# Kernel optimization log

Measured on AMD Instinct MI355X. Metric: run time of the kernel, lower is better.

## Reference

```python
import jax, jax.numpy as jnp
import numpy as np

N_NODES = 100000
N_EDGES = 1600000
D = 128


def gcn_conv(x, src, dst, ew, W, b, num_nodes):
    """PyG GCNConv: self-loops (weight 1), symmetric deg^{-1/2} normalization,
    linear transform (no bias) then scatter-add aggregation at dst, bias after."""
    loop = jnp.arange(num_nodes)
    s = jnp.concatenate([src, loop])
    d = jnp.concatenate([dst, loop])
    w = jnp.concatenate([ew, jnp.ones((num_nodes,), dtype=x.dtype)])
    deg = jax.ops.segment_sum(w, d, num_segments=num_nodes)
    dinv = jnp.where(deg > 0, jax.lax.rsqrt(deg), 0.0).astype(x.dtype)
    norm = dinv[s] * w * dinv[d]                      # [E+N]
    h = x @ W                                          # [N, out]
    msgs = h[s] * norm[:, None]                        # [E+N, out]
    return jax.ops.segment_sum(msgs, d, num_segments=num_nodes) + b


def setup_inputs() -> dict:
    key = jax.random.key(0)
    ks = jax.random.split(key, 7)
    x = jax.random.normal(ks[0], (N_NODES, D), dtype=jnp.float32)
    edge_index = jax.random.randint(ks[1], (2, N_EDGES), 0, N_NODES, dtype=jnp.int64)
    edge_weight = jax.random.uniform(ks[2], (N_EDGES,), dtype=jnp.float32)
    scale = 1.0 / np.sqrt(D)
    W1 = jax.random.normal(ks[3], (D, D), dtype=jnp.float32) * scale
    b1 = jax.random.normal(ks[4], (D,), dtype=jnp.float32) * 0.01
    W2 = jax.random.normal(ks[5], (D, D), dtype=jnp.float32) * scale
    b2 = jax.random.normal(ks[6], (D,), dtype=jnp.float32) * 0.01
    return {"x": x, "edge_index": edge_index, "edge_weight": edge_weight,
            "W1": W1, "b1": b1, "W2": W2, "b2": b2}


def reference(x, edge_index, edge_weight, W1, b1, W2, b2):
    src, dst = edge_index[0], edge_index[1]
    n = x.shape[0]
    h = gcn_conv(x, src, dst, edge_weight, W1, b1, n)
    h = jax.nn.relu(h)
    h = gcn_conv(h, src, dst, edge_weight, W2, b2, n)
    return jax.nn.relu(h)
```

## Files before the change

### kernel.cpp

```cpp
#include <hip/hip_runtime.h>

#define D 128
#define CAP 64
#define NCELL 391
#define BN2 256
#define CELLCAP 4608
#define BCAP 16
#define ABLK 768

typedef __attribute__((ext_vector_type(8))) short bf16x8;
typedef __attribute__((ext_vector_type(4))) float f32x4;
typedef __attribute__((ext_vector_type(4))) uint  u32x4;
typedef __attribute__((ext_vector_type(2))) float f32x2;

__device__ __forceinline__ ushort f2bf(float f) {
    uint u = __float_as_uint(f);
    return (ushort)((u + 0x7FFFu + ((u >> 16) & 1u)) >> 16);
}

__global__ __launch_bounds__(256) void k_prep(const float* __restrict__ W1,
                                              const float* __restrict__ W2,
                                              ushort* __restrict__ Wt1,
                                              ushort* __restrict__ Wt2,
                                              int* scnt) {
    int i = blockIdx.x * 256 + threadIdx.x;
    if (i < NCELL) scnt[i] = 0;
    if (i < 2 * D * D) {
        const float* W = (i < D * D) ? W1 : W2;
        ushort* Wt     = (i < D * D) ? Wt1 : Wt2;
        int j = i & (D * D - 1);
        int k = j >> 7, nn = j & 127;
        Wt[nn * D + k] = f2bf(W[k * D + nn]);
    }
}

__global__ __launch_bounds__(256) void k_bin(const int* __restrict__ src,
                                             const int* __restrict__ dst,
                                             const float* __restrict__ ew,
                                             int* scnt,
                                             uint2* __restrict__ rec, int nE, int epb) {
    __shared__ uint2 lrec[NCELL * BCAP];
    __shared__ int   bcnt[NCELL];
    __shared__ int   gbase[NCELL];
    const int tid = threadIdx.x;

    for (int i = tid; i < NCELL; i += 256) bcnt[i] = 0;
    __syncthreads();

    int e0 = blockIdx.x * epb;
    int e1 = min(e0 + epb, nE);
    for (int e = e0 + tid; e < e1; e += 256) {
        int d = dst[e];
        uint q = (uint)__float2int_rn(ew[e] * 32767.0f);
        uint2 r = make_uint2(((uint)src[e] << 15) | q, (uint)(d & (BN2 - 1)));
        int cell = d >> 8;
        int p = atomicAdd(&bcnt[cell], 1);
        if (p < BCAP) {
            lrec[cell * BCAP + p] = r;
        } else {
            int gp = atomicAdd(&scnt[cell], 1);
            if (gp < CELLCAP) rec[(size_t)cell * CELLCAP + gp] = r;
        }
    }
    __syncthreads();

    const int offs = (blockIdx.x * 97) % NCELL;

    for (int i = tid; i < NCELL; i += 256) {
        int cell = i + offs; if (cell >= NCELL) cell -= NCELL;
        int c = min(bcnt[cell], BCAP);
        gbase[cell] = (c > 0) ? atomicAdd(&scnt[cell], c) : 0;
    }
    __syncthreads();

    const int wave = tid >> 6, lane = tid & 63;
    for (int i = wave; i < NCELL; i += 4) {
        int cell = i + offs; if (cell >= NCELL) cell -= NCELL;
        int c = min(bcnt[cell], BCAP);
        if (lane < c)
            rec[(size_t)cell * CELLCAP + gbase[cell] + lane] = lrec[cell * BCAP + lane];
    }
}

__global__ __launch_bounds__(256) void k_build(const uint2* __restrict__ rec,
                                               const int* __restrict__ scnt,
                                               uint* __restrict__ bucket,
                                               int* __restrict__ cnt,
                                               float* __restrict__ dinv, int n) {
    __shared__ uint rows[BN2 * (CAP + 1)];
    __shared__ int  lcnt[BN2];
    const int tid = threadIdx.x;
    const int b   = blockIdx.x;

    lcnt[tid] = 0;
    __syncthreads();

    int c = min(scnt[b], CELLCAP);
    for (int i = tid; i < c; i += 256) {
        uint2 r = rec[(size_t)b * CELLCAP + i];
        int nl = (int)r.y;
        int p = atomicAdd(&lcnt[nl], 1);
        if (p < CAP - 1) rows[nl * (CAP + 1) + p] = r.x;
    }
    __syncthreads();

    int node = b * BN2 + tid;
    int cc = min(lcnt[tid], CAP - 1);
    lcnt[tid] = cc;
    if (node < n) {
        float wsum = 0.f;
        for (int i = 0; i < cc; ++i)
            wsum += (float)(rows[tid * (CAP + 1) + i] & 32767u);
        dinv[node] = rsqrtf(1.0f + wsum * (1.0f / 32767.0f));
        cnt[node]  = cc + 1;
    }
    __syncthreads();

    for (int i = tid; i < BN2 * CAP; i += 256) {
        int nl = i >> 6, sl = i & (CAP - 1);
        int nd = b * BN2 + nl;
        if (nd < n) {
            int ce = lcnt[nl];
            uint o = 0u;
            if (sl < ce)       o = rows[nl * (CAP + 1) + sl];
            else if (sl == ce) o = ((uint)nd << 15) | 32767u;
            bucket[(size_t)nd * CAP + sl] = o;
        }
    }
}

__global__ __launch_bounds__(256) void k_norm(uint* __restrict__ bucket,
                                              const int* __restrict__ cnt,
                                              const float* __restrict__ dinv, int n) {
    int node = blockIdx.x * 16 + (threadIdx.x >> 4);
    if (node >= n) return;
    int sl = threadIdx.x & 15;
    float dd = dinv[node];
    int c = cnt[node];
    uint* row = bucket + (size_t)node * CAP;
    for (int j = sl; j < c; j += 16) {
        uint e = row[j];
        uint s = e >> 15;
        float w = (float)(e & 32767u) * (1.0f / 32767.0f) * dinv[s] * dd;
        row[j] = (s << 15) | (uint)__float2int_rn(w * 32767.0f);
    }
}

template <bool IN_BF16>
__global__ __launch_bounds__(256) void k_gemm(const void* __restrict__ Xv,
                                              const ushort* __restrict__ Wt,
                                              ushort* __restrict__ H, int n) {
    __shared__ ushort Xs[64][136];
    __shared__ ushort Ws[128][136];
    const int tid  = threadIdx.x;
    const int row0 = blockIdx.x * 64;

#pragma unroll
    for (int p = 0; p < 8; ++p) {
        int f = (p * 256 + tid) * 8;
        int nn = f >> 7, kk = f & 127;
        *(uint4*)(&Ws[nn][kk]) = *(const uint4*)(Wt + f);
    }
    if (IN_BF16) {
        const ushort* X = (const ushort*)Xv;
#pragma unroll
        for (int p = 0; p < 4; ++p) {
            int f = (p * 256 + tid) * 8;
            int r = f >> 7, kk = f & 127;
            uint4 v = {0u, 0u, 0u, 0u};
            if (row0 + r < n) v = *(const uint4*)(X + (size_t)(row0 + r) * D + kk);
            *(uint4*)(&Xs[r][kk]) = v;
        }
    } else {
        const float* X = (const float*)Xv;
#pragma unroll
        for (int p = 0; p < 8; ++p) {
            int f = (p * 256 + tid) * 4;
            int r = f >> 7, kk = f & 127;
            float4 v = {0.f, 0.f, 0.f, 0.f};
            if (row0 + r < n) v = *(const float4*)(X + (size_t)(row0 + r) * D + kk);
            ushort4 o;
            o.x = f2bf(v.x); o.y = f2bf(v.y); o.z = f2bf(v.z); o.w = f2bf(v.w);
            *(ushort4*)(&Xs[r][kk]) = o;
        }
    }
    __syncthreads();

    const int lane = tid & 63;
    const int wave = tid >> 6;
    const int m    = lane & 15;
    const int quad = lane >> 4;
    const int rw   = wave * 16;

    f32x4 acc[8] = {};
#pragma unroll
    for (int kt = 0; kt < 4; ++kt) {
        int k0 = kt * 32 + quad * 8;
        bf16x8 a = *(const bf16x8*)(&Xs[rw + m][k0]);
#pragma unroll
        for (int t = 0; t < 8; ++t) {
            bf16x8 b = *(const bf16x8*)(&Ws[t * 16 + m][k0]);
            acc[t] = __builtin_amdgcn_mfma_f32_16x16x32_bf16(a, b, acc[t], 0, 0, 0);
        }
    }

#pragma unroll
    for (int t = 0; t < 8; ++t) {
#pragma unroll
        for (int r = 0; r < 4; ++r) {
            int row = row0 + rw + quad * 4 + r;
            if (row < n) H[(size_t)row * D + t * 16 + m] = f2bf(acc[t][r]);
        }
    }
}

template <bool OUT_BF16>
__global__ __launch_bounds__(256) void k_agg(const ushort* __restrict__ H,
                                             const int* __restrict__ cnt,
                                             const uint* __restrict__ bucket,
                                             const float* __restrict__ bias,
                                             void* __restrict__ outv, int n) {
    int node = blockIdx.x * 8 + (threadIdx.x >> 5);
    int l32  = threadIdx.x & 31;
    int nda  = min(node, n - 1);
    const uint2*  Hu2  = (const uint2*)H;
    const u32x4*  row4 = (const u32x4*)(bucket + (size_t)nda * CAP);

    int c = (node < n) ? cnt[node] : 0;
    int cmax = max(c, __shfl_xor(c, 32));

    f32x2 acc0 = {0.f, 0.f};
    f32x2 acc1 = {0.f, 0.f};
    for (int j = 0; j < cmax; j += 8) {
        u32x4 pa = __builtin_nontemporal_load(row4 + (j >> 2));
        u32x4 pb = __builtin_nontemporal_load(row4 + (j >> 2) + 1);
#pragma unroll
        for (int t = 0; t < 8; ++t) {
            uint p   = (t < 4) ? pa[t] : pb[t - 4];
            uint idx = ((p >> 10) & 0x003FFFE0u) | (uint)l32;
            uint2 h  = Hu2[idx];
            float w  = (float)(p & 32767u) * (1.0f / 32767.0f);
            f32x2 f0, f1;
            f0.x = __uint_as_float(h.x << 16);
            f0.y = __uint_as_float(h.x & 0xFFFF0000u);
            f1.x = __uint_as_float(h.y << 16);
            f1.y = __uint_as_float(h.y & 0xFFFF0000u);
            acc0 = f0 * w + acc0;
            acc1 = f1 * w + acc1;
        }
    }

    float4 bv = *(const float4*)(bias + l32 * 4);
    float r0 = fmaxf(acc0.x + bv.x, 0.f);
    float r1 = fmaxf(acc0.y + bv.y, 0.f);
    float r2 = fmaxf(acc1.x + bv.z, 0.f);
    float r3 = fmaxf(acc1.y + bv.w, 0.f);
    if (node < n) {
        if (OUT_BF16) {
            uint2 o;
            o.x = (uint)f2bf(r0) | ((uint)f2bf(r1) << 16);
            o.y = (uint)f2bf(r2) | ((uint)f2bf(r3) << 16);
            ((uint2*)outv)[(size_t)node * 32 + l32] = o;
        } else {
            f32x4 r = {r0, r1, r2, r3};
            __builtin_nontemporal_store(r, (f32x4*)outv + (size_t)node * 32 + l32);
        }
    }
}

extern "C" void kernel_launch(void* const* d_in, const int* in_sizes, int n_in,
                              void* d_out, int out_size, void* d_ws, size_t ws_size,
                              hipStream_t stream) {
    const float* x  = (const float*)d_in[0];
    const int*   ei = (const int*)d_in[1];
    const float* ew = (const float*)d_in[2];
    const float* W1 = (const float*)d_in[3];
    const float* b1 = (const float*)d_in[4];
    const float* W2 = (const float*)d_in[5];
    const float* b2 = (const float*)d_in[6];

    const int n  = in_sizes[0] / D;
    const int nE = in_sizes[2];
    const int* src = ei;
    const int* dst = ei + nE;

    float* out = (float*)d_out;

    uint2*  rec    = (uint2*)d_ws;
    uint*   bucket = (uint*)(rec + (size_t)NCELL * CELLCAP);
    ushort* Hbuf   = (ushort*)(bucket + (size_t)n * CAP);
    ushort* Abuf   = Hbuf + (size_t)n * D;
    ushort* Wt1    = Abuf + (size_t)n * D;
    ushort* Wt2    = Wt1 + D * D;
    float*  dinv   = (float*)(Wt2 + D * D);
    int*    cnt    = (int*)(dinv + n);
    int*    scnt   = cnt + n;

    const int epb      = (nE + ABLK - 1) / ABLK;
    const int nBlkAgg  = (n + 7) / 8;
    const int nBlkNorm = (n + 15) / 16;
    const int nBlkGemm = (n + 63) / 64;

    k_prep <<<128,      256, 0, stream>>>(W1, W2, Wt1, Wt2, scnt);
    k_bin  <<<ABLK,     256, 0, stream>>>(src, dst, ew, scnt, rec, nE, epb);
    k_build<<<NCELL,    256, 0, stream>>>(rec, scnt, bucket, cnt, dinv, n);
    k_norm <<<nBlkNorm, 256, 0, stream>>>(bucket, cnt, dinv, n);

    k_gemm<false><<<nBlkGemm, 256, 0, stream>>>(x, Wt1, Hbuf, n);
    k_agg<true>  <<<nBlkAgg,  256, 0, stream>>>(Hbuf, cnt, bucket, b1, Abuf, n);

    k_gemm<true> <<<nBlkGemm, 256, 0, stream>>>(Abuf, Wt2, Hbuf, n);
    k_agg<false> <<<nBlkAgg,  256, 0, stream>>>(Hbuf, cnt, bucket, b2, out, n);
}
```

Measured before the change: 346.4 us.

## Merge edge binning and first GEMM into one heterogeneous launch

Combines the edge-binning kernel and the layer-1 GEMM (fp32 input converted to bf16) into a single launch. Block IDs below ABLK do binning and the rest do GEMM tiles, so the independent work can overlap and one launch gap goes away. It also makes the binned-record stores and loads nontemporal to reduce cache pollution. The shared buffer is sized for the larger of the two roles, which may lower occupancy for the GEMM blocks.

```diff
diff --git a/kernel.cpp b/kernel.cpp
--- a/kernel.cpp
+++ b/kernel.cpp
@@ -11,6 +11,7 @@
 typedef __attribute__((ext_vector_type(8))) short bf16x8;
 typedef __attribute__((ext_vector_type(4))) float f32x4;
 typedef __attribute__((ext_vector_type(4))) uint  u32x4;
+typedef __attribute__((ext_vector_type(2))) uint  u32x2;
 typedef __attribute__((ext_vector_type(2))) float f32x2;
 
 __device__ __forceinline__ ushort f2bf(float f) {
@@ -34,51 +35,111 @@
     }
 }
 
-__global__ __launch_bounds__(256) void k_bin(const int* __restrict__ src,
-                                             const int* __restrict__ dst,
-                                             const float* __restrict__ ew,
-                                             int* scnt,
-                                             uint2* __restrict__ rec, int nE, int epb) {
-    __shared__ uint2 lrec[NCELL * BCAP];
-    __shared__ int   bcnt[NCELL];
-    __shared__ int   gbase[NCELL];
+__global__ __launch_bounds__(256) void k_bin_gemm(const int* __restrict__ src,
+                                                  const int* __restrict__ dst,
+                                                  const float* __restrict__ ew,
+                                                  int* scnt,
+                                                  uint2* __restrict__ rec, int nE, int epb,
+                                                  const float* __restrict__ X,
+                                                  const ushort* __restrict__ Wt,
+                                                  ushort* __restrict__ H, int n) {
+    __shared__ __align__(16) char smem[53248];
     const int tid = threadIdx.x;
 
-    for (int i = tid; i < NCELL; i += 256) bcnt[i] = 0;
-    __syncthreads();
-
-    int e0 = blockIdx.x * epb;
-    int e1 = min(e0 + epb, nE);
-    for (int e = e0 + tid; e < e1; e += 256) {
-        int d = dst[e];
-        uint q = (uint)__float2int_rn(ew[e] * 32767.0f);
-        uint2 r = make_uint2(((uint)src[e] << 15) | q, (uint)(d & (BN2 - 1)));
-        int cell = d >> 8;
-        int p = atomicAdd(&bcnt[cell], 1);
-        if (p < BCAP) {
-            lrec[cell * BCAP + p] = r;
-        } else {
-            int gp = atomicAdd(&scnt[cell], 1);
-            if (gp < CELLCAP) rec[(size_t)cell * CELLCAP + gp] = r;
-        }
-    }
-    __syncthreads();
-
-    const int offs = (blockIdx.x * 97) % NCELL;
-
-    for (int i = tid; i < NCELL; i += 256) {
-        int cell = i + offs; if (cell >= NCELL) cell -= NCELL;
-        int c = min(bcnt[cell], BCAP);
-        gbase[cell] = (c > 0) ? atomicAdd(&scnt[cell], c) : 0;
-    }
-    __syncthreads();
-
-    const int wave = tid >> 6, lane = tid & 63;
-    for (int i = wave; i < NCELL; i += 4) {
-        int cell = i + offs; if (cell >= NCELL) cell -= NCELL;
-        int c = min(bcnt[cell], BCAP);
-        if (lane < c)
-            rec[(size_t)cell * CELLCAP + gbase[cell] + lane] = lrec[cell * BCAP + lane];
+    if (blockIdx.x < ABLK) {
+        uint2* lrec  = (uint2*)smem;
+        int*   bcnt  = (int*)(smem + 50048);
+        int*   gbase = (int*)(smem + 50048 + 1564);
+
+        for (int i = tid; i < NCELL; i += 256) bcnt[i] = 0;
+        __syncthreads();
+
+        int e0 = blockIdx.x * epb;
+        int e1 = min(e0 + epb, nE);
+        for (int e = e0 + tid; e < e1; e += 256) {
+            int d = dst[e];
+            uint q = (uint)__float2int_rn(ew[e] * 32767.0f);
+            uint2 r = make_uint2(((uint)src[e] << 15) | q, (uint)(d & (BN2 - 1)));
+            int cell = d >> 8;
+            int p = atomicAdd(&bcnt[cell], 1);
+            if (p < BCAP) {
+                lrec[cell * BCAP + p] = r;
+            } else {
+                int gp = atomicAdd(&scnt[cell], 1);
+                if (gp < CELLCAP) rec[(size_t)cell * CELLCAP + gp] = r;
+            }
+        }
+        __syncthreads();
+
+        const int offs = (blockIdx.x * 97) % NCELL;
+
+        for (int i = tid; i < NCELL; i += 256) {
+            int cell = i + offs; if (cell >= NCELL) cell -= NCELL;
+            int c = min(bcnt[cell], BCAP);
+            gbase[cell] = (c > 0) ? atomicAdd(&scnt[cell], c) : 0;
+        }
+        __syncthreads();
+
+        const int wave = tid >> 6, lane = tid & 63;
+        for (int i = wave; i < NCELL; i += 4) {
+            int cell = i + offs; if (cell >= NCELL) cell -= NCELL;
+            int c = min(bcnt[cell], BCAP);
+            if (lane < c) {
+                uint2 v = lrec[cell * BCAP + lane];
+                u32x2 ve = {v.x, v.y};
+                __builtin_nontemporal_store(ve,
+                    (u32x2*)(rec + (size_t)cell * CELLCAP + gbase[cell] + lane));
+            }
+        }
+    } else {
+        ushort (*Xs)[136] = (ushort (*)[136])smem;
+        ushort (*Ws)[136] = (ushort (*)[136])(smem + 17408);
+        const int row0 = (blockIdx.x - ABLK) * 64;
+
+#pragma unroll
+        for (int p = 0; p < 8; ++p) {
+            int f = (p * 256 + tid) * 8;
+            int nn = f >> 7, kk = f & 127;
+            *(uint4*)(&Ws[nn][kk]) = *(const uint4*)(Wt + f);
+        }
+#pragma unroll
+        for (int p = 0; p < 8; ++p) {
+            int f = (p * 256 + tid) * 4;
+            int r = f >> 7, kk = f & 127;
+            float4 v = {0.f, 0.f, 0.f, 0.f};
+            if (row0 + r < n) v = *(const float4*)(X + (size_t)(row0 + r) * D + kk);
+            ushort4 o;
+            o.x = f2bf(v.x); o.y = f2bf(v.y); o.z = f2bf(v.z); o.w = f2bf(v.w);
+            *(ushort4*)(&Xs[r][kk]) = o;
+        }
+        __syncthreads();
+
+        const int lane = tid & 63;
+        const int wave = tid >> 6;
+        const int m    = lane & 15;
+        const int quad = lane >> 4;
+        const int rw   = wave * 16;
+
+        f32x4 acc[8] = {};
+#pragma unroll
+        for (int kt = 0; kt < 4; ++kt) {
+            int k0 = kt * 32 + quad * 8;
+            bf16x8 a = *(const bf16x8*)(&Xs[rw + m][k0]);
+#pragma unroll
+            for (int t = 0; t < 8; ++t) {
+                bf16x8 b = *(const bf16x8*)(&Ws[t * 16 + m][k0]);
+                acc[t] = __builtin_amdgcn_mfma_f32_16x16x32_bf16(a, b, acc[t], 0, 0, 0);
+            }
+        }
+
+#pragma unroll
+        for (int t = 0; t < 8; ++t) {
+#pragma unroll
+            for (int r = 0; r < 4; ++r) {
+                int row = row0 + rw + quad * 4 + r;
+                if (row < n) H[(size_t)row * D + t * 16 + m] = f2bf(acc[t][r]);
+            }
+        }
     }
 }
 
@@ -97,7 +158,7 @@
 
     int c = min(scnt[b], CELLCAP);
     for (int i = tid; i < c; i += 256) {
-        uint2 r = rec[(size_t)b * CELLCAP + i];
+        u32x2 r = __builtin_nontemporal_load((const u32x2*)(rec + (size_t)b * CELLCAP + i));
         int nl = (int)r.y;
         int p = atomicAdd(&lcnt[nl], 1);
         if (p < CAP - 1) rows[nl * (CAP + 1) + p] = r.x;
@@ -146,10 +207,9 @@
     }
 }
 
-template <bool IN_BF16>
-__global__ __launch_bounds__(256) void k_gemm(const void* __restrict__ Xv,
-                                              const ushort* __restrict__ Wt,
-                                              ushort* __restrict__ H, int n) {
+__global__ __launch_bounds__(256) void k_gemm_bf(const ushort* __restrict__ X,
+                                                 const ushort* __restrict__ Wt,
+                                                 ushort* __restrict__ H, int n) {
     __shared__ ushort Xs[64][136];
     __shared__ ushort Ws[128][136];
     const int tid  = threadIdx.x;
@@ -161,28 +221,13 @@
         int nn = f >> 7, kk = f & 127;
         *(uint4*)(&Ws[nn][kk]) = *(const uint4*)(Wt + f);
     }
-    if (IN_BF16) {
-        const ushort* X = (const ushort*)Xv;
-#pragma unroll
-        for (int p = 0; p < 4; ++p) {
-            int f = (p * 256 + tid) * 8;
-            int r = f >> 7, kk = f & 127;
-            uint4 v = {0u, 0u, 0u, 0u};
-            if (row0 + r < n) v = *(const uint4*)(X + (size_t)(row0 + r) * D + kk);
-            *(uint4*)(&Xs[r][kk]) = v;
-        }
-    } else {
-        const float* X = (const float*)Xv;
-#pragma unroll
-        for (int p = 0; p < 8; ++p) {
-            int f = (p * 256 + tid) * 4;
-            int r = f >> 7, kk = f & 127;
-            float4 v = {0.f, 0.f, 0.f, 0.f};
-            if (row0 + r < n) v = *(const float4*)(X + (size_t)(row0 + r) * D + kk);
-            ushort4 o;
-            o.x = f2bf(v.x); o.y = f2bf(v.y); o.z = f2bf(v.z); o.w = f2bf(v.w);
-            *(ushort4*)(&Xs[r][kk]) = o;
-        }
+#pragma unroll
+    for (int p = 0; p < 4; ++p) {
+        int f = (p * 256 + tid) * 8;
+        int r = f >> 7, kk = f & 127;
+        uint4 v = {0u, 0u, 0u, 0u};
+        if (row0 + r < n) v = *(const uint4*)(X + (size_t)(row0 + r) * D + kk);
+        *(uint4*)(&Xs[r][kk]) = v;
     }
     __syncthreads();
 
@@ -301,14 +346,14 @@
     const int nBlkNorm = (n + 15) / 16;
     const int nBlkGemm = (n + 63) / 64;
 
-    k_prep <<<128,      256, 0, stream>>>(W1, W2, Wt1, Wt2, scnt);
-    k_bin  <<<ABLK,     256, 0, stream>>>(src, dst, ew, scnt, rec, nE, epb);
-    k_build<<<NCELL,    256, 0, stream>>>(rec, scnt, bucket, cnt, dinv, n);
-    k_norm <<<nBlkNorm, 256, 0, stream>>>(bucket, cnt, dinv, n);
-
-    k_gemm<false><<<nBlkGemm, 256, 0, stream>>>(x, Wt1, Hbuf, n);
+    k_prep    <<<128,               256, 0, stream>>>(W1, W2, Wt1, Wt2, scnt);
+    k_bin_gemm<<<ABLK + nBlkGemm,   256, 0, stream>>>(src, dst, ew, scnt, rec, nE, epb,
+                                                      x, Wt1, Hbuf, n);
+    k_build   <<<NCELL,             256, 0, stream>>>(rec, scnt, bucket, cnt, dinv, n);
+    k_norm    <<<nBlkNorm,          256, 0, stream>>>(bucket, cnt, dinv, n);
+
     k_agg<true>  <<<nBlkAgg,  256, 0, stream>>>(Hbuf, cnt, bucket, b1, Abuf, n);
 
-    k_gemm<true> <<<nBlkGemm, 256, 0, stream>>>(Abuf, Wt2, Hbuf, n);
+    k_gemm_bf    <<<nBlkGemm, 256, 0, stream>>>(Abuf, Wt2, Hbuf, n);
     k_agg<false> <<<nBlkAgg,  256, 0, stream>>>(Hbuf, cnt, bucket, b2, out, n);
 }
```

After: 341.4 us. No clear change (-1.4%).
